# Kernel tuning notes

Measured on AMD Instinct MI355X. Metric: run time of the kernel, lower is better.

## Reference

```python
import jax, jax.numpy as jnp
import numpy as np

OFFSET = 1e-6   # undefined global in source; small positive stabilizer
COS_EPS = 1e-8  # F.cosine_similarity default eps

B, N, M = 128, 2048, 128


def setup_inputs() -> dict:
    key = jax.random.key(0)
    ks = jax.random.split(key, 9)
    return {
        "memory": jax.random.normal(ks[0], (B, N, M), jnp.float32),
        "k_t": jax.random.normal(ks[1], (B, M), jnp.float32),
        "beta_t": jax.random.uniform(ks[2], (B,), jnp.float32),
        "g_t": jax.random.uniform(ks[3], (B,), jnp.float32),
        "w_t_minus_1": jax.random.uniform(ks[4], (B, N), jnp.float32),
        "s_t": jax.random.uniform(ks[5], (B, 3), jnp.float32),
        "gamma_t": jax.random.uniform(ks[6], (B,), jnp.float32),
        "e_t": jax.random.uniform(ks[7], (B, M), jnp.float32),
        "a_t": jax.random.normal(ks[8], (B, M), jnp.float32),
    }


def reference(memory, k_t, beta_t, g_t, w_t_minus_1, s_t, gamma_t, e_t, a_t):
    # ---- content_addressing (faithful to source, incl. w_tilde_t = w_{t-1} quirk) ----
    mk = memory + OFFSET                     # [B,N,M]
    kk = k_t[:, None, :] + OFFSET            # [B,1,M]
    dot = jnp.sum(mk * kk, axis=-1)          # [B,N]
    nm = jnp.maximum(jnp.sqrt(jnp.sum(mk * mk, -1)), COS_EPS)            # [B,N]
    nk = jnp.maximum(jnp.sqrt(jnp.sum(kk * kk, -1)), COS_EPS)            # [B,1]
    K = dot / (nm * nk)                      # cosine similarity, [B,N]
    w_c = jax.nn.softmax(beta_t[:, None] * K, axis=1)                    # [B,N]
    w_g = g_t[:, None] * w_c + (1.0 - g_t[:, None]) * w_t_minus_1        # [B,N]
    w_pow = w_t_minus_1 ** gamma_t[:, None]                              # sharpening on w_{t-1}
    w_t = jnp.sum(w_pow, axis=1, keepdims=True) + OFFSET                 # [B,1]
    w_t = jnp.broadcast_to(w_t, w_t_minus_1.shape)                       # [B,N] (source .repeat)

    # ---- writing: rank-1 erase/add memory update ----
    erase = w_t[:, :, None] * e_t[:, None, :]                            # [B,N,M]
    M_new = memory * (1.0 - erase) + w_t[:, :, None] * a_t[:, None, :]   # [B,N,M]

    # ---- reading ----
    r_t = jnp.einsum('bn,bnm->bm', w_t, M_new)                           # [B,M]

    # single concatenated output so every chain stays live: [B, M + 2N]
    return jnp.concatenate([r_t, w_t, w_g], axis=1)
```

## Files before the change

kernel.cpp:

```cpp
#include <hip/hip_runtime.h>
#include <hip/hip_bf16.h>
#include <math.h>

#define BB 128
#define NN 2048
#define MM 128
#define ROWS 32
#define CHUNKS (NN / ROWS)
#define STRIDE (MM + 4)
#define OFFSET_EPS 1e-6f
#define COS_EPS 1e-8f

__global__ __launch_bounds__(256, 8) void pass_a(
    const float* __restrict__ memory, const float* __restrict__ k_t,
    const float* __restrict__ beta_t, const float* __restrict__ w_prev,
    const float* __restrict__ gamma_t,
    float* __restrict__ colsum_part, float* __restrict__ ex_buf,
    float* __restrict__ esum_part,   float* __restrict__ psum_part)
{
    __shared__ float tile[ROWS * STRIDE];
    __shared__ float ks[MM];
    __shared__ float s_col[8][MM];
    __shared__ float s_red[4];
    __shared__ float s_bon;
    __shared__ float s_epsK1;

    const int b     = blockIdx.x / CHUNKS;
    const int chunk = blockIdx.x % CHUNKS;
    const int r0    = chunk * ROWS;
    const int t     = threadIdx.x;

    if (t < 32) {
        float4 kv = *(const float4*)(k_t + b * MM + 4 * t);
        const float e0 = kv.x + OFFSET_EPS, e1 = kv.y + OFFSET_EPS,
                    e2 = kv.z + OFFSET_EPS, e3 = kv.w + OFFSET_EPS;
        *(float4*)&ks[4 * t] = make_float4(e0, e1, e2, e3);
        float s2 = e0 * e0 + e1 * e1 + e2 * e2 + e3 * e3;
        float s1 = e0 + e1 + e2 + e3;
        #pragma unroll
        for (int s = 16; s; s >>= 1) {
            s2 += __shfl_xor(s2, s);
            s1 += __shfl_xor(s1, s);
        }
        if (t == 0) {
            s_bon   = beta_t[b] / fmaxf(sqrtf(s2), COS_EPS);
            s_epsK1 = OFFSET_EPS * s1;
        }
    }

    if (t < 8) {
        float4 w = *(const float4*)(w_prev + b * NN + r0 + 4 * t);
        const float gamma = gamma_t[b];
        float p = __powf(w.x, gamma) + __powf(w.y, gamma) +
                  __powf(w.z, gamma) + __powf(w.w, gamma);
        #pragma unroll
        for (int s = 4; s; s >>= 1) p += __shfl_xor(p, s);
        if (t == 0) psum_part[chunk * BB + b] = p;
    }

    const float* src = memory + (size_t)(b * NN + r0) * MM;
    float cs0 = 0.f, cs1 = 0.f, cs2 = 0.f, cs3 = 0.f;
    #pragma unroll
    for (int i = 0; i < 4; ++i) {
        float4 v = *(const float4*)(src + i * 1024 + 4 * t);
        cs0 += v.x; cs1 += v.y; cs2 += v.z; cs3 += v.w;
        const int row = i * 8 + (t >> 5);
        const int col = (4 * t) & 127;
        *(float4*)&tile[row * STRIDE + col] = v;
    }
    *(float4*)&s_col[t >> 5][(4 * t) & 127] = make_float4(cs0, cs1, cs2, cs3);
    __syncthreads();

    const int r = t >> 3;
    const int h = t & 7;
    const float* vrow = &tile[r * STRIDE + h * 16];
    const float* krow = &ks[h * 16];
    float dot = 0.f, sq = 0.f, rs = 0.f;
    #pragma unroll
    for (int j = 0; j < 4; ++j) {
        float4 v = *(const float4*)(vrow + 4 * j);
        float4 k = *(const float4*)(krow + 4 * j);
        dot += v.x * k.x + v.y * k.y + v.z * k.z + v.w * k.w;
        sq  += v.x * v.x + v.y * v.y + v.z * v.z + v.w * v.w;
        rs  += v.x + v.y + v.z + v.w;
    }
    dot += __shfl_xor(dot, 1); dot += __shfl_xor(dot, 2); dot += __shfl_xor(dot, 4);
    sq  += __shfl_xor(sq, 1);  sq  += __shfl_xor(sq, 2);  sq  += __shfl_xor(sq, 4);
    rs  += __shfl_xor(rs, 1);  rs  += __shfl_xor(rs, 2);  rs  += __shfl_xor(rs, 4);

    float ex = 0.f;
    if (h == 0) {
        const float d   = dot + s_epsK1;
        const float nm2 = sq + 2.0f * OFFSET_EPS * rs
                          + (float)MM * OFFSET_EPS * OFFSET_EPS;
        const float sc  = d * s_bon / fmaxf(sqrtf(nm2), COS_EPS);
        ex = __expf(sc);
        ex_buf[b * NN + r0 + r] = ex;
    }
    float es = ex;
    #pragma unroll
    for (int s = 32; s; s >>= 1) es += __shfl_xor(es, s);
    if ((t & 63) == 0) s_red[t >> 6] = es;
    __syncthreads();
    if (t == 0)
        esum_part[chunk * BB + b] = s_red[0] + s_red[1] + s_red[2] + s_red[3];

    if (t < MM) {
        float v = 0.f;
        #pragma unroll
        for (int g = 0; g < 8; ++g) v += s_col[g][t];
        colsum_part[(size_t)chunk * (BB * MM) + b * MM + t] = v;
    }
}

__global__ __launch_bounds__(256) void pass_b(
    const float* __restrict__ ex_buf, const float* __restrict__ g_t,
    const float* __restrict__ w_prev, const float* __restrict__ e_t,
    const float* __restrict__ a_t,    const float* __restrict__ colsum_part,
    const float* __restrict__ esum_part, const float* __restrict__ psum_part,
    float* __restrict__ out)
{
    const int b    = blockIdx.x >> 1;
    const int half = blockIdx.x & 1;
    const int t    = threadIdx.x;
    __shared__ float s_inv, s_S;

    if (t < CHUNKS) {
        float es = esum_part[t * BB + b];
        float ps = psum_part[t * BB + b];
        #pragma unroll
        for (int s = 32; s; s >>= 1) {
            es += __shfl_xor(es, s);
            ps += __shfl_xor(ps, s);
        }
        if (t == 0) {
            s_inv = 1.f / es;
            s_S   = ps + OFFSET_EPS;
        }
    }
    __syncthreads();
    const float inv = s_inv, S = s_S, g = g_t[b];

    float* orow = out + (size_t)b * (MM + 2 * NN);
    const int n0 = half * 1024 + 4 * t;
    float4 ex4 = *(const float4*)(ex_buf + b * NN + n0);
    float4 w4  = *(const float4*)(w_prev + b * NN + n0);
    float4 wg;
    wg.x = g * ex4.x * inv + (1.f - g) * w4.x;
    wg.y = g * ex4.y * inv + (1.f - g) * w4.y;
    wg.z = g * ex4.z * inv + (1.f - g) * w4.z;
    wg.w = g * ex4.w * inv + (1.f - g) * w4.w;
    *(float4*)(orow + MM + n0)      = make_float4(S, S, S, S);
    *(float4*)(orow + MM + NN + n0) = wg;

    if (half == 0 && t < MM) {
        float cs = 0.f;
        #pragma unroll
        for (int c = 0; c < CHUNKS; ++c)
            cs += colsum_part[(size_t)c * (BB * MM) + b * MM + t];
        orow[t] = S * ((1.f - S * e_t[b * MM + t]) * cs +
                       (float)NN * S * a_t[b * MM + t]);
    }
}

extern "C" void kernel_launch(void* const* d_in, const int* in_sizes, int n_in,
                              void* d_out, int out_size, void* d_ws, size_t ws_size,
                              hipStream_t stream) {
    const float* memory  = (const float*)d_in[0];
    const float* k_t     = (const float*)d_in[1];
    const float* beta_t  = (const float*)d_in[2];
    const float* g_t     = (const float*)d_in[3];
    const float* w_prev  = (const float*)d_in[4];
    const float* gamma_t = (const float*)d_in[6];
    const float* e_t     = (const float*)d_in[7];
    const float* a_t     = (const float*)d_in[8];
    float* out = (float*)d_out;

    float* colsum_part = (float*)d_ws;
    float* ex_buf      = colsum_part + (size_t)CHUNKS * BB * MM;
    float* esum_part   = ex_buf + BB * NN;
    float* psum_part   = esum_part + CHUNKS * BB;

    pass_a<<<BB * CHUNKS, 256, 0, stream>>>(memory, k_t, beta_t, w_prev,
                                            gamma_t, colsum_part, ex_buf,
                                            esum_part, psum_part);
    pass_b<<<2 * BB, 256, 0, stream>>>(ex_buf, g_t, w_prev, e_t, a_t,
                                       colsum_part, esum_part, psum_part, out);
}
```

Measured before the change: 209.3 us.

## Compute row dot/norm from registers and double rows per block

Drops the shared-memory staging tile in pass_a, so each thread loads memory rows straight into registers and computes the dot product, squared norm and row sum there. Column sums are reduced with wave shuffles instead of shared memory. Rows per block go from 32 to 64, which halves the block count and the partial-sum buffers, and the pass_b reduction is shortened to match. This removes LDS round trips and a barrier, at the cost of more shuffle work and fewer blocks in flight.

```diff
diff --git a/kernel.cpp b/kernel.cpp
--- a/kernel.cpp
+++ b/kernel.cpp
@@ -1,26 +1,22 @@
 #include <hip/hip_runtime.h>
-#include <hip/hip_bf16.h>
 #include <math.h>
 
 #define BB 128
 #define NN 2048
 #define MM 128
-#define ROWS 32
+#define ROWS 64
 #define CHUNKS (NN / ROWS)
-#define STRIDE (MM + 4)
 #define OFFSET_EPS 1e-6f
 #define COS_EPS 1e-8f
 
-__global__ __launch_bounds__(256, 8) void pass_a(
+__global__ __launch_bounds__(256, 4) void pass_a(
     const float* __restrict__ memory, const float* __restrict__ k_t,
     const float* __restrict__ beta_t, const float* __restrict__ w_prev,
     const float* __restrict__ gamma_t,
     float* __restrict__ colsum_part, float* __restrict__ ex_buf,
     float* __restrict__ esum_part,   float* __restrict__ psum_part)
 {
-    __shared__ float tile[ROWS * STRIDE];
-    __shared__ float ks[MM];
-    __shared__ float s_col[8][MM];
+    __shared__ float s_col[4][MM];
     __shared__ float s_red[4];
     __shared__ float s_bon;
     __shared__ float s_epsK1;
@@ -29,12 +25,15 @@
     const int chunk = blockIdx.x % CHUNKS;
     const int r0    = chunk * ROWS;
     const int t     = threadIdx.x;
+    const int w     = t >> 6;
+    const int l     = t & 63;
+    const int h     = l & 7;
+    const int rr    = l >> 3;
 
     if (t < 32) {
         float4 kv = *(const float4*)(k_t + b * MM + 4 * t);
         const float e0 = kv.x + OFFSET_EPS, e1 = kv.y + OFFSET_EPS,
                     e2 = kv.z + OFFSET_EPS, e3 = kv.w + OFFSET_EPS;
-        *(float4*)&ks[4 * t] = make_float4(e0, e1, e2, e3);
         float s2 = e0 * e0 + e1 * e1 + e2 * e2 + e3 * e3;
         float s1 = e0 + e1 + e2 + e3;
         #pragma unroll
@@ -48,67 +47,91 @@
         }
     }
 
-    if (t < 8) {
-        float4 w = *(const float4*)(w_prev + b * NN + r0 + 4 * t);
+    if (t < 16) {
+        float4 wv = *(const float4*)(w_prev + b * NN + r0 + 4 * t);
         const float gamma = gamma_t[b];
-        float p = __powf(w.x, gamma) + __powf(w.y, gamma) +
-                  __powf(w.z, gamma) + __powf(w.w, gamma);
-        #pragma unroll
-        for (int s = 4; s; s >>= 1) p += __shfl_xor(p, s);
+        float p = __powf(wv.x, gamma) + __powf(wv.y, gamma) +
+                  __powf(wv.z, gamma) + __powf(wv.w, gamma);
+        #pragma unroll
+        for (int s = 8; s; s >>= 1) p += __shfl_xor(p, s);
         if (t == 0) psum_part[chunk * BB + b] = p;
     }
 
-    const float* src = memory + (size_t)(b * NN + r0) * MM;
-    float cs0 = 0.f, cs1 = 0.f, cs2 = 0.f, cs3 = 0.f;
-    #pragma unroll
-    for (int i = 0; i < 4; ++i) {
-        float4 v = *(const float4*)(src + i * 1024 + 4 * t);
-        cs0 += v.x; cs1 += v.y; cs2 += v.z; cs3 += v.w;
-        const int row = i * 8 + (t >> 5);
-        const int col = (4 * t) & 127;
-        *(float4*)&tile[row * STRIDE + col] = v;
-    }
-    *(float4*)&s_col[t >> 5][(4 * t) & 127] = make_float4(cs0, cs1, cs2, cs3);
+    float4 k4[4];
+    #pragma unroll
+    for (int j = 0; j < 4; ++j) {
+        float4 kv = *(const float4*)(k_t + b * MM + j * 32 + h * 4);
+        k4[j] = make_float4(kv.x + OFFSET_EPS, kv.y + OFFSET_EPS,
+                            kv.z + OFFSET_EPS, kv.w + OFFSET_EPS);
+    }
+
+    const float* src = memory + ((size_t)b * NN + r0 + w * 16) * MM;
+    float4 cs[4];
+    #pragma unroll
+    for (int j = 0; j < 4; ++j) cs[j] = make_float4(0.f, 0.f, 0.f, 0.f);
+    float d_[2], q_[2], r_[2];
+
+    #pragma unroll
+    for (int i = 0; i < 2; ++i) {
+        const float* p = src + (i * 8 + rr) * MM + h * 4;
+        float dot = 0.f, sq = 0.f, rs = 0.f;
+        #pragma unroll
+        for (int j = 0; j < 4; ++j) {
+            float4 v = *(const float4*)(p + j * 32);
+            dot += v.x * k4[j].x + v.y * k4[j].y +
+                   v.z * k4[j].z + v.w * k4[j].w;
+            sq  += v.x * v.x + v.y * v.y + v.z * v.z + v.w * v.w;
+            rs  += v.x + v.y + v.z + v.w;
+            cs[j].x += v.x; cs[j].y += v.y; cs[j].z += v.z; cs[j].w += v.w;
+        }
+        dot += __shfl_xor(dot, 1); dot += __shfl_xor(dot, 2); dot += __shfl_xor(dot, 4);
+        sq  += __shfl_xor(sq, 1);  sq  += __shfl_xor(sq, 2);  sq  += __shfl_xor(sq, 4);
+        rs  += __shfl_xor(rs, 1);  rs  += __shfl_xor(rs, 2);  rs  += __shfl_xor(rs, 4);
+        d_[i] = dot; q_[i] = sq; r_[i] = rs;
+    }
+
+    #pragma unroll
+    for (int j = 0; j < 4; ++j) {
+        #pragma unroll
+        for (int s = 8; s < 64; s <<= 1) {
+            cs[j].x += __shfl_xor(cs[j].x, s);
+            cs[j].y += __shfl_xor(cs[j].y, s);
+            cs[j].z += __shfl_xor(cs[j].z, s);
+            cs[j].w += __shfl_xor(cs[j].w, s);
+        }
+    }
+    if (l < 8) {
+        #pragma unroll
+        for (int j = 0; j < 4; ++j)
+            *(float4*)&s_col[w][l * 4 + j * 32] = cs[j];
+    }
     __syncthreads();
 
-    const int r = t >> 3;
-    const int h = t & 7;
-    const float* vrow = &tile[r * STRIDE + h * 16];
-    const float* krow = &ks[h * 16];
-    float dot = 0.f, sq = 0.f, rs = 0.f;
-    #pragma unroll
-    for (int j = 0; j < 4; ++j) {
-        float4 v = *(const float4*)(vrow + 4 * j);
-        float4 k = *(const float4*)(krow + 4 * j);
-        dot += v.x * k.x + v.y * k.y + v.z * k.z + v.w * k.w;
-        sq  += v.x * v.x + v.y * v.y + v.z * v.z + v.w * v.w;
-        rs  += v.x + v.y + v.z + v.w;
-    }
-    dot += __shfl_xor(dot, 1); dot += __shfl_xor(dot, 2); dot += __shfl_xor(dot, 4);
-    sq  += __shfl_xor(sq, 1);  sq  += __shfl_xor(sq, 2);  sq  += __shfl_xor(sq, 4);
-    rs  += __shfl_xor(rs, 1);  rs  += __shfl_xor(rs, 2);  rs  += __shfl_xor(rs, 4);
-
-    float ex = 0.f;
+    float exs = 0.f;
     if (h == 0) {
-        const float d   = dot + s_epsK1;
-        const float nm2 = sq + 2.0f * OFFSET_EPS * rs
-                          + (float)MM * OFFSET_EPS * OFFSET_EPS;
-        const float sc  = d * s_bon / fmaxf(sqrtf(nm2), COS_EPS);
-        ex = __expf(sc);
-        ex_buf[b * NN + r0 + r] = ex;
-    }
-    float es = ex;
-    #pragma unroll
-    for (int s = 32; s; s >>= 1) es += __shfl_xor(es, s);
-    if ((t & 63) == 0) s_red[t >> 6] = es;
+        const float bon   = s_bon;
+        const float epsK1 = s_epsK1;
+        #pragma unroll
+        for (int i = 0; i < 2; ++i) {
+            const float d   = d_[i] + epsK1;
+            const float nm2 = q_[i] + 2.0f * OFFSET_EPS * r_[i]
+                              + (float)MM * OFFSET_EPS * OFFSET_EPS;
+            const float sc  = d * bon / fmaxf(sqrtf(nm2), COS_EPS);
+            const float ex  = __expf(sc);
+            ex_buf[b * NN + r0 + w * 16 + i * 8 + rr] = ex;
+            exs += ex;
+        }
+    }
+    #pragma unroll
+    for (int s = 32; s; s >>= 1) exs += __shfl_xor(exs, s);
+    if (l == 0) s_red[w] = exs;
     __syncthreads();
+
     if (t == 0)
         esum_part[chunk * BB + b] = s_red[0] + s_red[1] + s_red[2] + s_red[3];
 
     if (t < MM) {
-        float v = 0.f;
-        #pragma unroll
-        for (int g = 0; g < 8; ++g) v += s_col[g][t];
+        const float v = s_col[0][t] + s_col[1][t] + s_col[2][t] + s_col[3][t];
         colsum_part[(size_t)chunk * (BB * MM) + b * MM + t] = v;
     }
 }
@@ -129,7 +152,7 @@
         float es = esum_part[t * BB + b];
         float ps = psum_part[t * BB + b];
         #pragma unroll
-        for (int s = 32; s; s >>= 1) {
+        for (int s = 16; s; s >>= 1) {
             es += __shfl_xor(es, s);
             ps += __shfl_xor(ps, s);
         }
```

New measurement: 209.3 us. No clear change (+0.0%).
